# Optimization experiments

Hardware: AMD Instinct MI355X
Metric: run time of the kernel (lower is better)

The kernel has to match this reference:

```python
import jax, jax.numpy as jnp
import numpy as np

CAUSAL = True


def setup_inputs() -> dict:
    key = jax.random.key(0)
    k1, k2, k3 = jax.random.split(key, 3)
    B, H, T, D = 2, 16, 2048, 64
    q = jax.random.normal(k1, (B, H, T, D), dtype=jnp.float32)
    k = jax.random.normal(k2, (B, H, T, D), dtype=jnp.float32)
    v = jax.random.normal(k3, (B, H, T, D), dtype=jnp.float32)
    return {"q": q, "k": k, "v": v}


def reference(q, k, v):
    # q,k,v: [B,H,T,D]
    d = q.shape[-1]
    scale = d ** -0.5
    dots = jnp.einsum('bhid,bhjd->bhij', q, k) * scale  # [B,H,T,T]
    if CAUSAL:
        t = q.shape[2]
        mask = jnp.triu(jnp.ones((t, t), dtype=bool), k=1)  # True above diagonal
        dots = jnp.where(mask, -jnp.inf, dots)
    attn = jax.nn.softmax(dots, axis=-1)
    # torch.einsum('bhjd,bhij->bhid', v, attn) == attn @ v
    return jnp.einsum('bhij,bhjd->bhid', attn, v)
```

## Files before the change

### kernel.cpp

```cpp
#include <hip/hip_runtime.h>
#include <hip/hip_bf16.h>

typedef unsigned short u16;
typedef unsigned int u32;
typedef __bf16 bf16x8 __attribute__((ext_vector_type(8)));
typedef u16 u16x8 __attribute__((ext_vector_type(8)));
typedef float floatx4 __attribute__((ext_vector_type(4)));

#define T_SEQ 2048
#define HDIM 64
#define NBH 32

static __device__ __forceinline__ u16 f2b_rne(float x) {
    union { float f; u32 u; } c; c.f = x;
    u32 u = c.u;
    return (u16)((u + 0x7fffu + ((u >> 16) & 1u)) >> 16);
}
static __device__ __forceinline__ u16 f2b_trunc(float x) {
    union { float f; u32 u; } c; c.f = x;
    return (u16)(c.u >> 16);
}

#define GLOAD_LDS16(gp, lp)                                                      \
    __builtin_amdgcn_global_load_lds(                                            \
        (const __attribute__((address_space(1))) u32*)(gp),                      \
        (__attribute__((address_space(3))) u32*)(lp), 16, 0, 0)

#define WAIT_VM(N) asm volatile("s_waitcnt vmcnt(" #N ")" ::: "memory")

__global__ __launch_bounds__(256) void prep(const float* __restrict__ k,
                                            const float* __restrict__ v,
                                            u16* __restrict__ kb,
                                            u16* __restrict__ vt) {
    __shared__ u16 tile[64][68];
    const int bh = blockIdx.y, t0 = blockIdx.x * 64;
    const int tid = threadIdx.x;

    const float* ksrc = k + ((size_t)bh * T_SEQ + t0) * HDIM;
    u16* kdst = kb + ((size_t)bh * T_SEQ + t0) * HDIM;
#pragma unroll
    for (int p = 0; p < 4; p++) {
        int idx = p * 256 + tid;
        float4 f = ((const float4*)ksrc)[idx];
        ushort4 o;
        o.x = f2b_rne(f.x); o.y = f2b_rne(f.y); o.z = f2b_rne(f.z); o.w = f2b_rne(f.w);
        ((ushort4*)kdst)[idx] = o;
    }

    const float* vsrc = v + ((size_t)bh * T_SEQ + t0) * HDIM;
#pragma unroll
    for (int p = 0; p < 4; p++) {
        int idx = p * 256 + tid;
        int r = idx >> 4, c4 = (idx & 15) * 4;
        float4 f = *(const float4*)(vsrc + r * HDIM + c4);
        tile[c4 + 0][r] = f2b_rne(f.x);
        tile[c4 + 1][r] = f2b_rne(f.y);
        tile[c4 + 2][r] = f2b_rne(f.z);
        tile[c4 + 3][r] = f2b_rne(f.w);
    }
    __syncthreads();
    u16* dst = vt + (size_t)bh * HDIM * T_SEQ + t0;
#pragma unroll
    for (int p = 0; p < 2; p++) {
        int idx = p * 256 + tid;
        int d = idx >> 3, pb = idx & 7;
        int k0 = (pb >> 2) * 32 + (pb & 3) * 4;
        union { u16x8 v8; ushort4 q[2]; } w;
        w.q[0] = *(ushort4*)&tile[d][k0];
        w.q[1] = *(ushort4*)&tile[d][k0 + 16];
        *(u16x8*)(dst + (size_t)d * T_SEQ + pb * 8) = w.v8;
    }
}

__global__ __launch_bounds__(512, 4) void fattn(const float* __restrict__ q,
                                                const u16* __restrict__ kb,
                                                const u16* __restrict__ vtb,
                                                float* __restrict__ out) {
    __shared__ __align__(16) u16 Kl[4][64 * 64];
    __shared__ __align__(16) u16 Vl[4][64 * 64];

    const int id = blockIdx.x;
    const int xcd = id & 7;
    const int u = id >> 3;
    const int bh = xcd * 4 + (u & 3);
    const int s = u >> 2;
    const int pr = (s & 8) ? (s ^ 7) : s;
    const int qtHi = 31 - pr, qtLo = pr;

    const int tid = threadIdx.x;
    const int wave = tid >> 6, lane = tid & 63;
    const int l15 = lane & 15, quad = lane >> 4;
    const int qt = (wave < 4) ? qtHi : qtLo;
    const int wrow = (wave & 3) * 16;
    const int qrow_base = qt * 64 + wrow;

    const float* qp = q + (size_t)bh * T_SEQ * HDIM;
    const u16* kp = kb + (size_t)bh * T_SEQ * HDIM;
    const u16* vp = vtb + (size_t)bh * HDIM * T_SEQ;

    const int srow = wave * 8 + (lane >> 3);
    const int slot = lane & 7;
    const u16* kg0 = kp + srow * HDIM + (slot ^ (srow & 7)) * 8;
    const u16* vg0 = vp + (size_t)srow * T_SEQ + ((slot - srow) & 7) * 8;

    auto stage = [&](int j, int buf) {
        GLOAD_LDS16(kg0 + j * 64 * HDIM, &Kl[buf][wave * 512]);
        GLOAD_LDS16(vg0 + j * 64, &Vl[buf][wave * 512]);
    };

    const float SL2E = 0.125f * 1.44269504088896f;
    bf16x8 qf[2];
    {
        const float* qrow = qp + (size_t)(qrow_base + l15) * HDIM;
#pragma unroll
        for (int kc = 0; kc < 2; kc++) {
            const float4* p4 = (const float4*)(qrow + kc * 32 + quad * 8);
            float4 fa = p4[0], fb = p4[1];
            union { bf16x8 v; u16 s[8]; } cv;
            cv.s[0] = f2b_rne(fa.x * SL2E); cv.s[1] = f2b_rne(fa.y * SL2E);
            cv.s[2] = f2b_rne(fa.z * SL2E); cv.s[3] = f2b_rne(fa.w * SL2E);
            cv.s[4] = f2b_rne(fb.x * SL2E); cv.s[5] = f2b_rne(fb.y * SL2E);
            cv.s[6] = f2b_rne(fb.z * SL2E); cv.s[7] = f2b_rne(fb.w * SL2E);
            qf[kc] = cv.v;
        }
    }

    stage(0, 0);
    stage(1, 1);
    stage(2, 2);

    floatx4 o_acc[4];
#pragma unroll
    for (int dt = 0; dt < 4; dt++) o_acc[dt] = (floatx4){0.f, 0.f, 0.f, 0.f};
    float ls0 = 0.f, ls1 = 0.f;

    for (int j = 0; j <= qtHi; ++j) {
        if (j + 2 <= qtHi)      WAIT_VM(4);
        else if (j + 1 <= qtHi) WAIT_VM(2);
        else                    WAIT_VM(0);
        __builtin_amdgcn_s_barrier();

        if (j + 3 <= qtHi) stage(j + 3, (j + 3) & 3);
        if (j > qt) continue;

        const int cur = j & 3;

        floatx4 sacc[4];
#pragma unroll
        for (int t = 0; t < 4; t++) sacc[t] = (floatx4){0.f, 0.f, 0.f, 0.f};
        const u16* Kc = Kl[cur];
        __builtin_amdgcn_s_setprio(1);
#pragma unroll
        for (int kc = 0; kc < 2; kc++) {
#pragma unroll
            for (int t = 0; t < 4; t++) {
                int rk = t * 16 + l15;
                bf16x8 kf = *(const bf16x8*)(Kc + rk * 64 + ((kc * 4 + quad) ^ (rk & 7)) * 8);
                sacc[t] = __builtin_amdgcn_mfma_f32_16x16x32_bf16(kf, qf[kc], sacc[t], 0, 0, 0);
            }
        }
        __builtin_amdgcn_s_setprio(0);

        union { bf16x8 v; u16 h[8]; } pk[2];
        const bool diag = (j == qt);
        const int gq = wrow + l15;
#pragma unroll
        for (int t = 0; t < 4; t++) {
#pragma unroll
            for (int rg = 0; rg < 4; rg++) {
                float e = __builtin_amdgcn_exp2f(sacc[t][rg]);
                if (diag && (t * 16 + quad * 4 + rg > gq)) e = 0.f;
                if (t < 2) ls0 += e; else ls1 += e;
                pk[t >> 1].h[(t & 1) * 4 + rg] = f2b_trunc(e);
            }
        }

        const u16* Vc = Vl[cur];
        __builtin_amdgcn_s_setprio(1);
#pragma unroll
        for (int tp = 0; tp < 2; tp++) {
#pragma unroll
            for (int dt = 0; dt < 4; dt++) {
                int d = dt * 16 + l15;
                int sl = (tp * 4 + quad + d) & 7;
                bf16x8 vf = *(const bf16x8*)(Vc + d * 64 + sl * 8);
                o_acc[dt] = __builtin_amdgcn_mfma_f32_16x16x32_bf16(pk[tp].v, vf, o_acc[dt], 0, 0, 0);
            }
        }
        __builtin_amdgcn_s_setprio(0);
    }

    float tot = ls0 + ls1;
    tot += __shfl_xor(tot, 16, 64);
    tot += __shfl_xor(tot, 32, 64);
    float* op = out + (size_t)bh * T_SEQ * HDIM;
#pragma unroll
    for (int rg = 0; rg < 4; rg++) {
        float inv = 1.0f / __shfl(tot, quad * 4 + rg, 64);
        size_t row = (size_t)(qrow_base + quad * 4 + rg) * HDIM;
#pragma unroll
        for (int dt = 0; dt < 4; dt++)
            op[row + dt * 16 + l15] = o_acc[dt][rg] * inv;
    }
}

extern "C" void kernel_launch(void* const* d_in, const int* in_sizes, int n_in,
                              void* d_out, int out_size, void* d_ws, size_t ws_size,
                              hipStream_t stream) {
    const float* q = (const float*)d_in[0];
    const float* k = (const float*)d_in[1];
    const float* v = (const float*)d_in[2];
    float* out = (float*)d_out;

    u16* kb = (u16*)d_ws;
    u16* vt = kb + (size_t)NBH * T_SEQ * HDIM;

    prep<<<dim3(T_SEQ / 64, NBH), 256, 0, stream>>>(k, v, kb, vt);
    fattn<<<dim3(512), 512, 0, stream>>>(q, kb, vt, out);
}
```

Baseline: 123.1 us.

## Split key block across wave pairs with 32-row query tiles and LDS reduction

Each wave now owns 32 query rows and half of each 64-key block (instead of 16 rows and all keys), so every K fragment loaded from LDS feeds two MFMAs and each V fragment feeds two. This reduces LDS read traffic per MFMA. Row sums are computed with an MFMA against a ones vector instead of scalar adds and shuffles. K fragments are loaded before the next tile's prefetch is issued. The two key-halves are combined at the end through an LDS exchange, at the cost of extra barriers, more accumulator registers and half the waves sitting idle during the epilogue.

```diff
diff --git a/kernel.cpp b/kernel.cpp
--- a/kernel.cpp
+++ b/kernel.cpp
@@ -90,9 +90,11 @@
     const int tid = threadIdx.x;
     const int wave = tid >> 6, lane = tid & 63;
     const int l15 = lane & 15, quad = lane >> 4;
-    const int qt = (wave < 4) ? qtHi : qtLo;
-    const int wrow = (wave & 3) * 16;
-    const int qrow_base = qt * 64 + wrow;
+    const int tile_sel = wave >> 2;
+    const int qhalf = (wave >> 1) & 1;
+    const int khalf = wave & 1;
+    const int qt = tile_sel ? qtLo : qtHi;
+    const int qrow_base = qt * 64 + qhalf * 32;
 
     const float* qp = q + (size_t)bh * T_SEQ * HDIM;
     const u16* kp = kb + (size_t)bh * T_SEQ * HDIM;
@@ -109,30 +111,42 @@
     };
 
     const float SL2E = 0.125f * 1.44269504088896f;
-    bf16x8 qf[2];
+    bf16x8 qf[2][2];
     {
-        const float* qrow = qp + (size_t)(qrow_base + l15) * HDIM;
-#pragma unroll
-        for (int kc = 0; kc < 2; kc++) {
-            const float4* p4 = (const float4*)(qrow + kc * 32 + quad * 8);
-            float4 fa = p4[0], fb = p4[1];
-            union { bf16x8 v; u16 s[8]; } cv;
-            cv.s[0] = f2b_rne(fa.x * SL2E); cv.s[1] = f2b_rne(fa.y * SL2E);
-            cv.s[2] = f2b_rne(fa.z * SL2E); cv.s[3] = f2b_rne(fa.w * SL2E);
-            cv.s[4] = f2b_rne(fb.x * SL2E); cv.s[5] = f2b_rne(fb.y * SL2E);
-            cv.s[6] = f2b_rne(fb.z * SL2E); cv.s[7] = f2b_rne(fb.w * SL2E);
-            qf[kc] = cv.v;
-        }
-    }
+#pragma unroll
+        for (int qb = 0; qb < 2; qb++) {
+            const float* qrow = qp + (size_t)(qrow_base + qb * 16 + l15) * HDIM;
+#pragma unroll
+            for (int kc = 0; kc < 2; kc++) {
+                const float4* p4 = (const float4*)(qrow + kc * 32 + quad * 8);
+                float4 fa = p4[0], fb = p4[1];
+                union { bf16x8 v; u16 s[8]; } cv;
+                cv.s[0] = f2b_rne(fa.x * SL2E); cv.s[1] = f2b_rne(fa.y * SL2E);
+                cv.s[2] = f2b_rne(fa.z * SL2E); cv.s[3] = f2b_rne(fa.w * SL2E);
+                cv.s[4] = f2b_rne(fb.x * SL2E); cv.s[5] = f2b_rne(fb.y * SL2E);
+                cv.s[6] = f2b_rne(fb.z * SL2E); cv.s[7] = f2b_rne(fb.w * SL2E);
+                qf[qb][kc] = cv.v;
+            }
+        }
+    }
+
+    union { u16 h[8]; bf16x8 v; } onesu;
+#pragma unroll
+    for (int i = 0; i < 8; i++) onesu.h[i] = 0x3F80;
+    const bf16x8 ones = onesu.v;
 
     stage(0, 0);
     stage(1, 1);
     stage(2, 2);
 
-    floatx4 o_acc[4];
-#pragma unroll
-    for (int dt = 0; dt < 4; dt++) o_acc[dt] = (floatx4){0.f, 0.f, 0.f, 0.f};
-    float ls0 = 0.f, ls1 = 0.f;
+    floatx4 o_acc[2][4];
+    floatx4 lsacc[2];
+#pragma unroll
+    for (int qb = 0; qb < 2; qb++) {
+        lsacc[qb] = (floatx4){0.f, 0.f, 0.f, 0.f};
+#pragma unroll
+        for (int dt = 0; dt < 4; dt++) o_acc[qb][dt] = (floatx4){0.f, 0.f, 0.f, 0.f};
+    }
 
     for (int j = 0; j <= qtHi; ++j) {
         if (j + 2 <= qtHi)      WAIT_VM(4);
@@ -140,67 +154,116 @@
         else                    WAIT_VM(0);
         __builtin_amdgcn_s_barrier();
 
+        const int cur = j & 3;
+        const bool active = (j <= qt);
+
+        bf16x8 kf[2][2];
+        if (active) {
+            const u16* Kc = Kl[cur];
+#pragma unroll
+            for (int kc = 0; kc < 2; kc++)
+#pragma unroll
+                for (int kb2 = 0; kb2 < 2; kb2++) {
+                    int rk = khalf * 32 + kb2 * 16 + l15;
+                    kf[kc][kb2] = *(const bf16x8*)(Kc + rk * 64 + ((kc * 4 + quad) ^ (rk & 7)) * 8);
+                }
+        }
         if (j + 3 <= qtHi) stage(j + 3, (j + 3) & 3);
-        if (j > qt) continue;
-
-        const int cur = j & 3;
-
-        floatx4 sacc[4];
-#pragma unroll
-        for (int t = 0; t < 4; t++) sacc[t] = (floatx4){0.f, 0.f, 0.f, 0.f};
-        const u16* Kc = Kl[cur];
+        if (!active) continue;
+
+        floatx4 sacc[2][2];
+#pragma unroll
+        for (int kb2 = 0; kb2 < 2; kb2++)
+#pragma unroll
+            for (int qb = 0; qb < 2; qb++) sacc[kb2][qb] = (floatx4){0.f, 0.f, 0.f, 0.f};
         __builtin_amdgcn_s_setprio(1);
 #pragma unroll
-        for (int kc = 0; kc < 2; kc++) {
-#pragma unroll
-            for (int t = 0; t < 4; t++) {
-                int rk = t * 16 + l15;
-                bf16x8 kf = *(const bf16x8*)(Kc + rk * 64 + ((kc * 4 + quad) ^ (rk & 7)) * 8);
-                sacc[t] = __builtin_amdgcn_mfma_f32_16x16x32_bf16(kf, qf[kc], sacc[t], 0, 0, 0);
+        for (int kc = 0; kc < 2; kc++)
+#pragma unroll
+            for (int kb2 = 0; kb2 < 2; kb2++)
+#pragma unroll
+                for (int qb = 0; qb < 2; qb++)
+                    sacc[kb2][qb] = __builtin_amdgcn_mfma_f32_16x16x32_bf16(
+                        kf[kc][kb2], qf[qb][kc], sacc[kb2][qb], 0, 0, 0);
+        __builtin_amdgcn_s_setprio(0);
+
+        union { bf16x8 v; u16 h[8]; } pk[2];
+        if (j == qt) {
+            const int key0 = khalf * 32 + quad * 4;
+#pragma unroll
+            for (int qb = 0; qb < 2; qb++) {
+                const int gq = qhalf * 32 + qb * 16 + l15;
+#pragma unroll
+                for (int kb2 = 0; kb2 < 2; kb2++)
+#pragma unroll
+                    for (int rg = 0; rg < 4; rg++) {
+                        float e = __builtin_amdgcn_exp2f(sacc[kb2][qb][rg]);
+                        if (key0 + kb2 * 16 + rg > gq) e = 0.f;
+                        pk[qb].h[kb2 * 4 + rg] = f2b_trunc(e);
+                    }
             }
-        }
+        } else {
+#pragma unroll
+            for (int qb = 0; qb < 2; qb++)
+#pragma unroll
+                for (int kb2 = 0; kb2 < 2; kb2++)
+#pragma unroll
+                    for (int rg = 0; rg < 4; rg++)
+                        pk[qb].h[kb2 * 4 + rg] =
+                            f2b_trunc(__builtin_amdgcn_exp2f(sacc[kb2][qb][rg]));
+        }
+
+        const u16* Vc = Vl[cur];
+        bf16x8 vf[4];
+#pragma unroll
+        for (int dt = 0; dt < 4; dt++) {
+            int d = dt * 16 + l15;
+            vf[dt] = *(const bf16x8*)(Vc + d * 64 + ((khalf * 4 + quad + d) & 7) * 8);
+        }
+
+        __builtin_amdgcn_s_setprio(1);
+#pragma unroll
+        for (int dt = 0; dt < 4; dt++)
+#pragma unroll
+            for (int qb = 0; qb < 2; qb++)
+                o_acc[qb][dt] = __builtin_amdgcn_mfma_f32_16x16x32_bf16(
+                    pk[qb].v, vf[dt], o_acc[qb][dt], 0, 0, 0);
+        lsacc[0] = __builtin_amdgcn_mfma_f32_16x16x32_bf16(pk[0].v, ones, lsacc[0], 0, 0, 0);
+        lsacc[1] = __builtin_amdgcn_mfma_f32_16x16x32_bf16(pk[1].v, ones, lsacc[1], 0, 0, 0);
         __builtin_amdgcn_s_setprio(0);
-
-        union { bf16x8 v; u16 h[8]; } pk[2];
-        const bool diag = (j == qt);
-        const int gq = wrow + l15;
-#pragma unroll
-        for (int t = 0; t < 4; t++) {
+    }
+
+    __syncthreads();
+    const int r = wave >> 1;
+    float* xch = ((r & 2) ? (float*)&Vl[0][0] : (float*)&Kl[0][0]) + (r & 1) * 2560;
+    floatx4* xv = (floatx4*)xch;
+    if (khalf == 0) {
+#pragma unroll
+        for (int qb = 0; qb < 2; qb++)
+#pragma unroll
+            for (int dt = 0; dt < 4; dt++) xv[(qb * 4 + dt) * 64 + lane] = o_acc[qb][dt];
+        xv[8 * 64 + lane] = lsacc[0];
+        xv[9 * 64 + lane] = lsacc[1];
+    }
+    __syncthreads();
+    if (khalf == 1) {
+#pragma unroll
+        for (int qb = 0; qb < 2; qb++) {
+#pragma unroll
+            for (int dt = 0; dt < 4; dt++) o_acc[qb][dt] += xv[(qb * 4 + dt) * 64 + lane];
+            lsacc[qb] += xv[(8 + qb) * 64 + lane];
+        }
+        float* op = out + (size_t)bh * T_SEQ * HDIM;
+#pragma unroll
+        for (int qb = 0; qb < 2; qb++)
 #pragma unroll
             for (int rg = 0; rg < 4; rg++) {
-                float e = __builtin_amdgcn_exp2f(sacc[t][rg]);
-                if (diag && (t * 16 + quad * 4 + rg > gq)) e = 0.f;
-                if (t < 2) ls0 += e; else ls1 += e;
-                pk[t >> 1].h[(t & 1) * 4 + rg] = f2b_trunc(e);
+                float inv = 1.0f / lsacc[qb][rg];
+                size_t row = (size_t)(qrow_base + qb * 16 + quad * 4 + rg) * HDIM;
+#pragma unroll
+                for (int dt = 0; dt < 4; dt++)
+                    op[row + dt * 16 + l15] = o_acc[qb][dt][rg] * inv;
             }
-        }
-
-        const u16* Vc = Vl[cur];
-        __builtin_amdgcn_s_setprio(1);
-#pragma unroll
-        for (int tp = 0; tp < 2; tp++) {
-#pragma unroll
-            for (int dt = 0; dt < 4; dt++) {
-                int d = dt * 16 + l15;
-                int sl = (tp * 4 + quad + d) & 7;
-                bf16x8 vf = *(const bf16x8*)(Vc + d * 64 + sl * 8);
-                o_acc[dt] = __builtin_amdgcn_mfma_f32_16x16x32_bf16(pk[tp].v, vf, o_acc[dt], 0, 0, 0);
-            }
-        }
-        __builtin_amdgcn_s_setprio(0);
-    }
-
-    float tot = ls0 + ls1;
-    tot += __shfl_xor(tot, 16, 64);
-    tot += __shfl_xor(tot, 32, 64);
-    float* op = out + (size_t)bh * T_SEQ * HDIM;
-#pragma unroll
-    for (int rg = 0; rg < 4; rg++) {
-        float inv = 1.0f / __shfl(tot, quad * 4 + rg, 64);
-        size_t row = (size_t)(qrow_base + quad * 4 + rg) * HDIM;
-#pragma unroll
-        for (int dt = 0; dt < 4; dt++)
-            op[row + dt * 16 + l15] = o_acc[dt][rg] * inv;
     }
 }
 
```

Result: faster. 119.5 us (-2.9%).
